# Optimization experiments

Hardware: AMD Instinct MI355X
Metric: run time of the kernel (lower is better)

Reference implementation:

```python
import jax, jax.numpy as jnp
import numpy as np

K = 4      # number of per-slot Linear layers (self.k)
H = 512    # hidden_dim
B = 4      # branching factor at every tree level (B >= K -> no padded slots)
T = 1024   # number of trees (roots)
D = 3      # pooled tree levels (= idx_matrix.shape[1] - 2)
N0 = T * B ** D  # 65536 leaves


def _make_level(n_in):
    """Replicates the torch order_matrix / pooling construction for groups of size B.
    order[m, i] = group_base + (pos_in_group + m) % B, then +1 for the zero pad row.
    seg[i] = group id (torch.repeat_interleave of counts)."""
    i = np.arange(n_in)
    base = (i // B) * B
    pos = i % B
    m = np.arange(K)[:, None]
    order = base[None, :] + (pos[None, :] + m) % B + 1  # [K, n_in], all valid since B >= K
    seg = i // B
    return order.astype(np.int32), seg.astype(np.int32)


def setup_inputs() -> dict:
    key = jax.random.key(0)
    ks = jax.random.split(key, 5)
    x = jax.random.normal(ks[0], (N0, H), jnp.float32)
    node_idx = jnp.arange(N0, dtype=jnp.int32)  # idx_matrix[:, -1]
    o1, s1 = _make_level(N0)
    o2, s2 = _make_level(N0 // B)
    o3, s3 = _make_level(N0 // B // B)
    Wz = jax.random.normal(ks[1], (K, H, H), jnp.float32) / np.sqrt(H)   # k slot Linears
    bz = jax.random.normal(ks[2], (K, H), jnp.float32) * 0.02
    Wzf = jax.random.normal(ks[3], (H, H), jnp.float32) / np.sqrt(H)     # z_final_layer
    bzf = jax.random.normal(ks[4], (H,), jnp.float32) * 0.02
    return dict(x=x, Wz=Wz, bz=bz, Wzf=Wzf, bzf=bzf, node_idx=node_idx,
                order1=jnp.asarray(o1), order2=jnp.asarray(o2), order3=jnp.asarray(o3),
                seg1=jnp.asarray(s1), seg2=jnp.asarray(s2), seg3=jnp.asarray(s3))


def _tree_layer(data, order, seg, num_seg, Wz, bz, Wzf, bzf):
    # prepend zero row so padded entries (order == 0) gather zeros
    padded = jnp.concatenate([jnp.zeros((1, data.shape[-1]), data.dtype), data], axis=0)
    emb = padded[order]                                    # [K, N, H] gather
    emb = jnp.einsum('knh,kjh->nkj', emb, Wz) + bz[None]   # per-slot Linear (x @ W.T + b)
    emb = jnp.where((order.T == 0)[..., None], jnp.zeros((), emb.dtype), emb)  # mask padded slots
    emb = emb.sum(axis=1)                                  # sum over K slots -> [N, H]
    emb = emb @ Wzf.T + bzf                                # z_final_layer
    return jax.ops.segment_sum(emb, seg, num_segments=num_seg)  # global_add_pool


def reference(x, Wz, bz, Wzf, bzf, node_idx, order1, order2, order3, seg1, seg2, seg3):
    data = x[node_idx]
    for order, seg in ((order1, seg1), (order2, seg2), (order3, seg3)):
        data = _tree_layer(data, order, seg, order.shape[1] // B, Wz, bz, Wzf, bzf)
    return data  # [T, H]
```

## Files before the change

### kernel.cpp

```cpp
#include <hip/hip_runtime.h>


#define HD 512
#define LDA_T 34
#define LDB_T 68

struct GemmSmem {
    float As[2][32][LDA_T];
    float Bs[2][32][LDB_T];
};

template<int MODE>
__device__ __forceinline__
void gemm_tile(const float* __restrict__ A, const float* __restrict__ B,
               float* __restrict__ C, const float* __restrict__ bias,
               float bscale, int i0, int j0, GemmSmem& sm) {
    const int tid  = threadIdx.x;
    const int tx   = tid & 15, ty = tid >> 4;
    const int arow = tid >> 3, acol4 = (tid & 7) << 2;
    const int ntcol = tid & 63, ntkq = (tid >> 6) << 3;
    const int nncol4 = (tid & 15) << 2, nnk = tid >> 4;

    float4 apre, bpre0, bpre1;

    auto load_tiles = [&](int k0) {
        apre = *(const float4*)&A[(size_t)(i0 + arow) * HD + k0 + acol4];
        if (MODE == 2) {
            const float* bp = &B[(size_t)(j0 + ntcol) * HD + k0 + ntkq];
            bpre0 = *(const float4*)bp;
            bpre1 = *(const float4*)(bp + 4);
        } else if (MODE == 0) {
            bpre0 = *(const float4*)&B[(size_t)(k0 + nnk) * HD + j0 + nncol4];
            bpre1 = *(const float4*)&B[(size_t)(k0 + nnk + 16) * HD + j0 + nncol4];
        } else {
            const float* b0 = &B[(size_t)(k0 + nnk) * HD + j0 + nncol4];
            const float* b1 = &B[(size_t)(k0 + nnk + 16) * HD + j0 + nncol4];
            float4 s0 = *(const float4*)b0, s1 = *(const float4*)b1;
            #pragma unroll
            for (int q = 1; q < 4; ++q) {
                float4 t0 = *(const float4*)(b0 + q * 262144);
                float4 t1 = *(const float4*)(b1 + q * 262144);
                s0.x += t0.x; s0.y += t0.y; s0.z += t0.z; s0.w += t0.w;
                s1.x += t1.x; s1.y += t1.y; s1.z += t1.z; s1.w += t1.w;
            }
            bpre0 = s0; bpre1 = s1;
        }
    };
    auto store_tiles = [&](int buf) {
        sm.As[buf][acol4 + 0][arow] = apre.x;
        sm.As[buf][acol4 + 1][arow] = apre.y;
        sm.As[buf][acol4 + 2][arow] = apre.z;
        sm.As[buf][acol4 + 3][arow] = apre.w;
        if (MODE == 2) {
            sm.Bs[buf][ntkq + 0][ntcol] = bpre0.x;
            sm.Bs[buf][ntkq + 1][ntcol] = bpre0.y;
            sm.Bs[buf][ntkq + 2][ntcol] = bpre0.z;
            sm.Bs[buf][ntkq + 3][ntcol] = bpre0.w;
            sm.Bs[buf][ntkq + 4][ntcol] = bpre1.x;
            sm.Bs[buf][ntkq + 5][ntcol] = bpre1.y;
            sm.Bs[buf][ntkq + 6][ntcol] = bpre1.z;
            sm.Bs[buf][ntkq + 7][ntcol] = bpre1.w;
        } else {
            *(float4*)&sm.Bs[buf][nnk][nncol4]      = bpre0;
            *(float4*)&sm.Bs[buf][nnk + 16][nncol4] = bpre1;
        }
    };

    float acc[2][4] = {};
    load_tiles(0);
    store_tiles(0);
    __syncthreads();

    for (int t = 0; t < 16; ++t) {
        if (t < 15) load_tiles((t + 1) << 5);
        const int cur = t & 1;
        #pragma unroll
        for (int kk = 0; kk < 32; ++kk) {
            float2 av = *(const float2*)&sm.As[cur][kk][ty << 1];
            float4 bv = *(const float4*)&sm.Bs[cur][kk][tx << 2];
            acc[0][0] += av.x * bv.x; acc[0][1] += av.x * bv.y;
            acc[0][2] += av.x * bv.z; acc[0][3] += av.x * bv.w;
            acc[1][0] += av.y * bv.x; acc[1][1] += av.y * bv.y;
            acc[1][2] += av.y * bv.z; acc[1][3] += av.y * bv.w;
        }
        if (t < 15) {
            store_tiles(1 - cur);
            __syncthreads();
        }
    }

    float4 bv = make_float4(0.f, 0.f, 0.f, 0.f);
    if (bias) {
        float4 tb = *(const float4*)&bias[j0 + (tx << 2)];
        bv.x = bscale * tb.x; bv.y = bscale * tb.y;
        bv.z = bscale * tb.z; bv.w = bscale * tb.w;
    }
    #pragma unroll
    for (int r = 0; r < 2; ++r) {
        const int row = i0 + (ty << 1) + r;
        float4 o;
        o.x = acc[r][0] + bv.x; o.y = acc[r][1] + bv.y;
        o.z = acc[r][2] + bv.z; o.w = acc[r][3] + bv.w;
        *(float4*)&C[(size_t)row * HD + j0 + (tx << 2)] = o;
    }
}

__global__ __launch_bounds__(256) void pool_kernel(const float* __restrict__ x,
                                                   float* __restrict__ P3) {
    __shared__ float4 red[128];
    const int tree = blockIdx.x, tid = threadIdx.x;
    const float4* xp = (const float4*)x + (size_t)tree * 8192 + tid;
    float4 a0 = make_float4(0.f, 0.f, 0.f, 0.f), a1 = a0;
    #pragma unroll
    for (int g = 0; g < 4; ++g) {
        float4 v[8];
        #pragma unroll
        for (int i = 0; i < 8; ++i) v[i] = xp[(size_t)(g * 8 + i) * 256];
        #pragma unroll
        for (int i = 0; i < 8; i += 2) {
            a0.x += v[i].x;     a0.y += v[i].y;
            a0.z += v[i].z;     a0.w += v[i].w;
            a1.x += v[i + 1].x; a1.y += v[i + 1].y;
            a1.z += v[i + 1].z; a1.w += v[i + 1].w;
        }
    }
    a0.x += a1.x; a0.y += a1.y; a0.z += a1.z; a0.w += a1.w;
    if (tid >= 128) red[tid - 128] = a0;
    __syncthreads();
    if (tid < 128) {
        float4 b = red[tid];
        a0.x += b.x; a0.y += b.y; a0.z += b.z; a0.w += b.w;
        ((float4*)P3)[tree * 128 + tid] = a0;
    }
}

__global__ __launch_bounds__(256) void pre_kernel(
        const float* __restrict__ Wz, const float* __restrict__ Wzf,
        const float* __restrict__ bz, const float* __restrict__ bzf,
        float* __restrict__ M, float* __restrict__ c0) {
    __shared__ GemmSmem sm;
    const int b = blockIdx.x, tid = threadIdx.x;
    if (b < 128) {
        gemm_tile<1>(Wzf, Wz, M, nullptr, 0.f, (b >> 3) << 5, (b & 7) << 6, sm);
    } else {
        const int bb = b - 128, wave = tid >> 6, lane = tid & 63;
        const int hb = lane << 3;
        float4 s0 = *(const float4*)&bz[hb];
        float4 s1 = *(const float4*)&bz[hb + 4];
        #pragma unroll
        for (int q = 1; q < 4; ++q) {
            float4 t0 = *(const float4*)&bz[q * HD + hb];
            float4 t1 = *(const float4*)&bz[q * HD + hb + 4];
            s0.x += t0.x; s0.y += t0.y; s0.z += t0.z; s0.w += t0.w;
            s1.x += t1.x; s1.y += t1.y; s1.z += t1.z; s1.w += t1.w;
        }
        #pragma unroll
        for (int q = 0; q < 4; ++q) {
            const int j = bb * 16 + wave * 4 + q;
            const float4* wr = (const float4*)&Wzf[(size_t)j * HD + hb];
            float4 w0 = wr[0], w1 = wr[1];
            float p = w0.x * s0.x + w0.y * s0.y + w0.z * s0.z + w0.w * s0.w
                    + w1.x * s1.x + w1.y * s1.y + w1.z * s1.z + w1.w * s1.w;
            #pragma unroll
            for (int off = 32; off > 0; off >>= 1) p += __shfl_down(p, off);
            if (lane == 0) c0[j] = 4.f * (p + bzf[j]);
        }
    }
}

__global__ __launch_bounds__(256) void k_stage2(
        const float* __restrict__ M, const float* __restrict__ P3,
        const float* __restrict__ c0,
        float* __restrict__ M2, float* __restrict__ Y1, float* __restrict__ u) {
    __shared__ GemmSmem sm;
    const int b = blockIdx.x, tid = threadIdx.x;
    if (b < 128) {
        gemm_tile<0>(M, M, M2, nullptr, 0.f, (b >> 3) << 5, (b & 7) << 6, sm);
    } else if (b < 384) {
        const int bb = b - 128;
        gemm_tile<2>(P3, M, Y1, c0, 16.f, (bb >> 3) << 5, (bb & 7) << 6, sm);
    } else {
        const int bb = b - 384, wave = tid >> 6, lane = tid & 63;
        const int j = bb * 4 + wave, hb = lane << 3;
        const float4* mr = (const float4*)&M[(size_t)j * HD + hb];
        const float4* cr = (const float4*)&c0[hb];
        float4 m0 = mr[0], m1 = mr[1], q0 = cr[0], q1 = cr[1];
        float p = m0.x * q0.x + m0.y * q0.y + m0.z * q0.z + m0.w * q0.w
                + m1.x * q1.x + m1.y * q1.y + m1.z * q1.z + m1.w * q1.w;
        #pragma unroll
        for (int off = 32; off > 0; off >>= 1) p += __shfl_down(p, off);
        if (lane == 0) u[j] = 4.f * p + c0[j];
    }
}

__global__ __launch_bounds__(256) void k_stage3(
        const float* __restrict__ Y1, const float* __restrict__ M2,
        const float* __restrict__ u, float* __restrict__ out) {
    __shared__ GemmSmem sm;
    const int b = blockIdx.x;
    gemm_tile<2>(Y1, M2, out, u, 1.f, (b >> 3) << 5, (b & 7) << 6, sm);
}

extern "C" void kernel_launch(void* const* d_in, const int* in_sizes, int n_in,
                              void* d_out, int out_size, void* d_ws, size_t ws_size,
                              hipStream_t stream) {
    const float* x   = (const float*)d_in[0];
    const float* Wz  = (const float*)d_in[1];
    const float* bz  = (const float*)d_in[2];
    const float* Wzf = (const float*)d_in[3];
    const float* bzf = (const float*)d_in[4];
    float* out = (float*)d_out;

    float* ws = (float*)d_ws;
    float* P3 = ws;
    float* Y1 = ws + 524288;
    float* M  = ws + 1048576;
    float* M2 = ws + 1310720;
    float* c0 = ws + 1572864;
    float* u  = ws + 1573376;

    hipLaunchKernelGGL(pool_kernel, dim3(1024), dim3(256), 0, stream, x, P3);
    hipLaunchKernelGGL(pre_kernel,  dim3(160),  dim3(256), 0, stream,
                       Wz, Wzf, bz, bzf, M, c0);
    hipLaunchKernelGGL(k_stage2,    dim3(512),  dim3(256), 0, stream,
                       M, P3, c0, M2, Y1, u);
    hipLaunchKernelGGL(k_stage3,    dim3(256),  dim3(256), 0, stream,
                       Y1, M2, u, out);
}
```

Baseline: 314.4 us.

## Merge pooling and weight precompute into one launch and enlarge GEMM tiles to 64x64

Folds the leaf-pooling kernel into the first-stage kernel next to the Wzf·Wz GEMM and c0 blocks, dropping one kernel launch and letting these independent pieces run concurrently. GEMM tiles grow from 32x64 to 64x64 with a 4x4 per-thread micro-tile, raising arithmetic intensity per shared-memory load. The cost is fewer blocks in the GEMM stages (128 for the last stage) and higher register pressure, which may reduce occupancy on a chip with many CUs.

New measurement: 296.6 us. -5.7%, faster.

```diff
diff --git a/kernel.cpp b/kernel.cpp
--- a/kernel.cpp
+++ b/kernel.cpp
@@ -2,12 +2,11 @@
 
 
 #define HD 512
-#define LDA_T 34
-#define LDB_T 68
+#define LDT 68
 
 struct GemmSmem {
-    float As[2][32][LDA_T];
-    float Bs[2][32][LDB_T];
+    float As[2][32][LDT];
+    float Bs[2][32][LDT];
 };
 
 template<int MODE>
@@ -17,24 +16,25 @@
                float bscale, int i0, int j0, GemmSmem& sm) {
     const int tid  = threadIdx.x;
     const int tx   = tid & 15, ty = tid >> 4;
-    const int arow = tid >> 3, acol4 = (tid & 7) << 2;
-    const int ntcol = tid & 63, ntkq = (tid >> 6) << 3;
-    const int nncol4 = (tid & 15) << 2, nnk = tid >> 4;
-
-    float4 apre, bpre0, bpre1;
+    const int arow = tid >> 2, akq = (tid & 3) << 2;
+    const int bk   = tid >> 4, bc4 = (tid & 15) << 2;
+
+    float4 ap0, ap1, bp0, bp1;
 
     auto load_tiles = [&](int k0) {
-        apre = *(const float4*)&A[(size_t)(i0 + arow) * HD + k0 + acol4];
+        const float* ar = &A[(size_t)(i0 + arow) * HD + k0 + akq];
+        ap0 = *(const float4*)ar;
+        ap1 = *(const float4*)(ar + 16);
         if (MODE == 2) {
-            const float* bp = &B[(size_t)(j0 + ntcol) * HD + k0 + ntkq];
-            bpre0 = *(const float4*)bp;
-            bpre1 = *(const float4*)(bp + 4);
+            const float* br = &B[(size_t)(j0 + arow) * HD + k0 + akq];
+            bp0 = *(const float4*)br;
+            bp1 = *(const float4*)(br + 16);
         } else if (MODE == 0) {
-            bpre0 = *(const float4*)&B[(size_t)(k0 + nnk) * HD + j0 + nncol4];
-            bpre1 = *(const float4*)&B[(size_t)(k0 + nnk + 16) * HD + j0 + nncol4];
+            bp0 = *(const float4*)&B[(size_t)(k0 + bk) * HD + j0 + bc4];
+            bp1 = *(const float4*)&B[(size_t)(k0 + bk + 16) * HD + j0 + bc4];
         } else {
-            const float* b0 = &B[(size_t)(k0 + nnk) * HD + j0 + nncol4];
-            const float* b1 = &B[(size_t)(k0 + nnk + 16) * HD + j0 + nncol4];
+            const float* b0 = &B[(size_t)(k0 + bk) * HD + j0 + bc4];
+            const float* b1 = b0 + 16 * HD;
             float4 s0 = *(const float4*)b0, s1 = *(const float4*)b1;
             #pragma unroll
             for (int q = 1; q < 4; ++q) {
@@ -43,30 +43,34 @@
                 s0.x += t0.x; s0.y += t0.y; s0.z += t0.z; s0.w += t0.w;
                 s1.x += t1.x; s1.y += t1.y; s1.z += t1.z; s1.w += t1.w;
             }
-            bpre0 = s0; bpre1 = s1;
+            bp0 = s0; bp1 = s1;
         }
     };
     auto store_tiles = [&](int buf) {
-        sm.As[buf][acol4 + 0][arow] = apre.x;
-        sm.As[buf][acol4 + 1][arow] = apre.y;
-        sm.As[buf][acol4 + 2][arow] = apre.z;
-        sm.As[buf][acol4 + 3][arow] = apre.w;
+        sm.As[buf][akq + 0][arow]  = ap0.x;
+        sm.As[buf][akq + 1][arow]  = ap0.y;
+        sm.As[buf][akq + 2][arow]  = ap0.z;
+        sm.As[buf][akq + 3][arow]  = ap0.w;
+        sm.As[buf][akq + 16][arow] = ap1.x;
+        sm.As[buf][akq + 17][arow] = ap1.y;
+        sm.As[buf][akq + 18][arow] = ap1.z;
+        sm.As[buf][akq + 19][arow] = ap1.w;
         if (MODE == 2) {
-            sm.Bs[buf][ntkq + 0][ntcol] = bpre0.x;
-            sm.Bs[buf][ntkq + 1][ntcol] = bpre0.y;
-            sm.Bs[buf][ntkq + 2][ntcol] = bpre0.z;
-            sm.Bs[buf][ntkq + 3][ntcol] = bpre0.w;
-            sm.Bs[buf][ntkq + 4][ntcol] = bpre1.x;
-            sm.Bs[buf][ntkq + 5][ntcol] = bpre1.y;
-            sm.Bs[buf][ntkq + 6][ntcol] = bpre1.z;
-            sm.Bs[buf][ntkq + 7][ntcol] = bpre1.w;
+            sm.Bs[buf][akq + 0][arow]  = bp0.x;
+            sm.Bs[buf][akq + 1][arow]  = bp0.y;
+            sm.Bs[buf][akq + 2][arow]  = bp0.z;
+            sm.Bs[buf][akq + 3][arow]  = bp0.w;
+            sm.Bs[buf][akq + 16][arow] = bp1.x;
+            sm.Bs[buf][akq + 17][arow] = bp1.y;
+            sm.Bs[buf][akq + 18][arow] = bp1.z;
+            sm.Bs[buf][akq + 19][arow] = bp1.w;
         } else {
-            *(float4*)&sm.Bs[buf][nnk][nncol4]      = bpre0;
-            *(float4*)&sm.Bs[buf][nnk + 16][nncol4] = bpre1;
+            *(float4*)&sm.Bs[buf][bk][bc4]      = bp0;
+            *(float4*)&sm.Bs[buf][bk + 16][bc4] = bp1;
         }
     };
 
-    float acc[2][4] = {};
+    float acc[4][4] = {};
     load_tiles(0);
     store_tiles(0);
     __syncthreads();
@@ -76,12 +80,15 @@
         const int cur = t & 1;
         #pragma unroll
         for (int kk = 0; kk < 32; ++kk) {
-            float2 av = *(const float2*)&sm.As[cur][kk][ty << 1];
+            float4 av = *(const float4*)&sm.As[cur][kk][ty << 2];
             float4 bv = *(const float4*)&sm.Bs[cur][kk][tx << 2];
-            acc[0][0] += av.x * bv.x; acc[0][1] += av.x * bv.y;
-            acc[0][2] += av.x * bv.z; acc[0][3] += av.x * bv.w;
-            acc[1][0] += av.y * bv.x; acc[1][1] += av.y * bv.y;
-            acc[1][2] += av.y * bv.z; acc[1][3] += av.y * bv.w;
+            float aa[4] = {av.x, av.y, av.z, av.w};
+            float bb[4] = {bv.x, bv.y, bv.z, bv.w};
+            #pragma unroll
+            for (int i = 0; i < 4; ++i)
+                #pragma unroll
+                for (int j = 0; j < 4; ++j)
+                    acc[i][j] += aa[i] * bb[j];
         }
         if (t < 15) {
             store_tiles(1 - cur);
@@ -96,8 +103,8 @@
         bv.z = bscale * tb.z; bv.w = bscale * tb.w;
     }
     #pragma unroll
-    for (int r = 0; r < 2; ++r) {
-        const int row = i0 + (ty << 1) + r;
+    for (int r = 0; r < 4; ++r) {
+        const int row = i0 + (ty << 2) + r;
         float4 o;
         o.x = acc[r][0] + bv.x; o.y = acc[r][1] + bv.y;
         o.z = acc[r][2] + bv.z; o.w = acc[r][3] + bv.w;
@@ -105,10 +112,10 @@
     }
 }
 
-__global__ __launch_bounds__(256) void pool_kernel(const float* __restrict__ x,
-                                                   float* __restrict__ P3) {
-    __shared__ float4 red[128];
-    const int tree = blockIdx.x, tid = threadIdx.x;
+__device__ __forceinline__
+void pool_body(const float* __restrict__ x, float* __restrict__ P3,
+               int tree, float4* red) {
+    const int tid = threadIdx.x;
     const float4* xp = (const float4*)x + (size_t)tree * 8192 + tid;
     float4 a0 = make_float4(0.f, 0.f, 0.f, 0.f), a1 = a0;
     #pragma unroll
@@ -134,17 +141,20 @@
     }
 }
 
-__global__ __launch_bounds__(256) void pre_kernel(
-        const float* __restrict__ Wz, const float* __restrict__ Wzf,
-        const float* __restrict__ bz, const float* __restrict__ bzf,
-        float* __restrict__ M, float* __restrict__ c0) {
+__global__ __launch_bounds__(256) void k_stage1(
+        const float* __restrict__ x, const float* __restrict__ Wz,
+        const float* __restrict__ Wzf, const float* __restrict__ bz,
+        const float* __restrict__ bzf,
+        float* __restrict__ P3, float* __restrict__ M, float* __restrict__ c0) {
     __shared__ GemmSmem sm;
     const int b = blockIdx.x, tid = threadIdx.x;
-    if (b < 128) {
-        gemm_tile<1>(Wzf, Wz, M, nullptr, 0.f, (b >> 3) << 5, (b & 7) << 6, sm);
+    if (b < 64) {
+        gemm_tile<1>(Wzf, Wz, M, nullptr, 0.f, (b >> 3) << 6, (b & 7) << 6, sm);
+    } else if (b < 1088) {
+        pool_body(x, P3, b - 64, (float4*)&sm);
     } else {
-        const int bb = b - 128, wave = tid >> 6, lane = tid & 63;
-        const int hb = lane << 3;
+        const int j = (b - 1088) * 4 + (tid >> 6);
+        const int lane = tid & 63, hb = lane << 3;
         float4 s0 = *(const float4*)&bz[hb];
         float4 s1 = *(const float4*)&bz[hb + 4];
         #pragma unroll
@@ -154,17 +164,13 @@
             s0.x += t0.x; s0.y += t0.y; s0.z += t0.z; s0.w += t0.w;
             s1.x += t1.x; s1.y += t1.y; s1.z += t1.z; s1.w += t1.w;
         }
-        #pragma unroll
-        for (int q = 0; q < 4; ++q) {
-            const int j = bb * 16 + wave * 4 + q;
-            const float4* wr = (const float4*)&Wzf[(size_t)j * HD + hb];
-            float4 w0 = wr[0], w1 = wr[1];
-            float p = w0.x * s0.x + w0.y * s0.y + w0.z * s0.z + w0.w * s0.w
-                    + w1.x * s1.x + w1.y * s1.y + w1.z * s1.z + w1.w * s1.w;
-            #pragma unroll
-            for (int off = 32; off > 0; off >>= 1) p += __shfl_down(p, off);
-            if (lane == 0) c0[j] = 4.f * (p + bzf[j]);
-        }
+        const float4* wr = (const float4*)&Wzf[(size_t)j * HD + hb];
+        float4 w0 = wr[0], w1 = wr[1];
+        float p = w0.x * s0.x + w0.y * s0.y + w0.z * s0.z + w0.w * s0.w
+                + w1.x * s1.x + w1.y * s1.y + w1.z * s1.z + w1.w * s1.w;
+        #pragma unroll
+        for (int off = 32; off > 0; off >>= 1) p += __shfl_down(p, off);
+        if (lane == 0) c0[j] = 4.f * (p + bzf[j]);
     }
 }
 
@@ -175,13 +181,13 @@
     __shared__ GemmSmem sm;
     const int b = blockIdx.x, tid = threadIdx.x;
     if (b < 128) {
-        gemm_tile<0>(M, M, M2, nullptr, 0.f, (b >> 3) << 5, (b & 7) << 6, sm);
-    } else if (b < 384) {
+        gemm_tile<2>(P3, M, Y1, c0, 16.f, (b >> 3) << 6, (b & 7) << 6, sm);
+    } else if (b < 192) {
         const int bb = b - 128;
-        gemm_tile<2>(P3, M, Y1, c0, 16.f, (bb >> 3) << 5, (bb & 7) << 6, sm);
+        gemm_tile<0>(M, M, M2, nullptr, 0.f, (bb >> 3) << 6, (bb & 7) << 6, sm);
     } else {
-        const int bb = b - 384, wave = tid >> 6, lane = tid & 63;
-        const int j = bb * 4 + wave, hb = lane << 3;
+        const int j = (b - 192) * 4 + (tid >> 6);
+        const int lane = tid & 63, hb = lane << 3;
         const float4* mr = (const float4*)&M[(size_t)j * HD + hb];
         const float4* cr = (const float4*)&c0[hb];
         float4 m0 = mr[0], m1 = mr[1], q0 = cr[0], q1 = cr[1];
@@ -198,7 +204,7 @@
         const float* __restrict__ u, float* __restrict__ out) {
     __shared__ GemmSmem sm;
     const int b = blockIdx.x;
-    gemm_tile<2>(Y1, M2, out, u, 1.f, (b >> 3) << 5, (b & 7) << 6, sm);
+    gemm_tile<2>(Y1, M2, out, u, 1.f, (b >> 3) << 6, (b & 7) << 6, sm);
 }
 
 extern "C" void kernel_launch(void* const* d_in, const int* in_sizes, int n_in,
@@ -219,11 +225,10 @@
     float* c0 = ws + 1572864;
     float* u  = ws + 1573376;
 
-    hipLaunchKernelGGL(pool_kernel, dim3(1024), dim3(256), 0, stream, x, P3);
-    hipLaunchKernelGGL(pre_kernel,  dim3(160),  dim3(256), 0, stream,
-                       Wz, Wzf, bz, bzf, M, c0);
-    hipLaunchKernelGGL(k_stage2,    dim3(512),  dim3(256), 0, stream,
+    hipLaunchKernelGGL(k_stage1, dim3(1216), dim3(256), 0, stream,
+                       x, Wz, Wzf, bz, bzf, P3, M, c0);
+    hipLaunchKernelGGL(k_stage2, dim3(320), dim3(256), 0, stream,
                        M, P3, c0, M2, Y1, u);
-    hipLaunchKernelGGL(k_stage3,    dim3(256),  dim3(256), 0, stream,
+    hipLaunchKernelGGL(k_stage3, dim3(128), dim3(256), 0, stream,
                        Y1, M2, u, out);
 }
```
